# Kernel tuning notes

Measured on AMD Instinct MI355X. Metric: run time of the kernel, lower is better.

## Reference

```python
import jax, jax.numpy as jnp
import numpy as np

S_SCALE = 64.0   # arcface scale
MARGIN = 0.5     # arcface additive angular margin
EMB = 512
NUM_CLASSES = 100000
BATCH = 512


def setup_inputs() -> dict:
    key = jax.random.key(0)
    k1, k2, k3, k4 = jax.random.split(key, 4)
    # xavier_uniform for [num_classes, emb]
    limit = float(np.sqrt(6.0 / (NUM_CLASSES + EMB)))
    weight = jax.random.uniform(k1, (NUM_CLASSES, EMB), jnp.float32, -limit, limit)
    fc_weight = jax.random.uniform(k2, (NUM_CLASSES, EMB), jnp.float32, -limit, limit)
    local_embeddings = jax.random.normal(k3, (BATCH, EMB), jnp.float32)
    local_labels = jax.random.randint(k4, (BATCH,), 0, NUM_CLASSES, jnp.int64)
    return {
        "local_embeddings": local_embeddings,
        "weight": weight,
        "fc_weight": fc_weight,
        "local_labels": local_labels,
        "epoch": 40,
    }


def _l2norm(x, eps=1e-12):
    return x / jnp.maximum(jnp.linalg.norm(x, axis=-1, keepdims=True), eps)


def _arcface(logits, labels):
    # insightface ArcFace: replace target cosine with cos(theta + m), then scale by s
    rows = jnp.arange(logits.shape[0])
    target = logits[rows, labels]
    sin = jnp.sqrt(jnp.maximum(1.0 - target * target, 0.0))
    cos_m, sin_m = jnp.cos(MARGIN), jnp.sin(MARGIN)
    with_margin = target * cos_m - sin * sin_m            # cos(theta + m)
    # safeguard: only apply when theta + m <= pi  (target > cos(pi - m))
    threshold = jnp.cos(jnp.pi - MARGIN)
    mm = jnp.sin(jnp.pi - MARGIN) * MARGIN
    new_target = jnp.where(target > threshold, with_margin, target - mm)
    logits = logits.at[rows, labels].set(new_target)
    return logits * S_SCALE


def _ce(logits, labels):
    rows = jnp.arange(logits.shape[0])
    logp = jax.nn.log_softmax(logits, axis=-1)
    return -jnp.mean(logp[rows, labels])


def reference(local_embeddings, weight, fc_weight, local_labels, epoch):
    labels = local_labels.astype(jnp.int32)
    # margin branch: normalize both sides, cosine logits, arcface margin, CE
    norm_emb = _l2norm(local_embeddings)
    norm_w = _l2norm(weight)
    logits = norm_emb @ norm_w.T                   # [B, num_classes]
    logits = _arcface(logits, labels)
    margin_loss = _ce(logits, labels)
    # plain CE branch on raw linear
    ce_logits = local_embeddings @ fc_weight.T     # [B, num_classes]
    ce_loss = _ce(ce_logits, labels)
    if epoch <= 30:
        return ce_loss + 0.0 * margin_loss
    else:
        return 0.0 * ce_loss + margin_loss
```

## Files before the change

### kernel.cpp

```cpp
#include <hip/hip_runtime.h>

typedef __bf16 bf16x8 __attribute__((ext_vector_type(8)));
typedef float floatx4 __attribute__((ext_vector_type(4)));
typedef unsigned short ushortx8 __attribute__((ext_vector_type(8)));
typedef unsigned short ushort_t;

#define NC      100000
#define NCP     100096
#define EMBD    512
#define BATCH   512
#define BM      256
#define BN      128
#define BK      32
#define NCH     782

#define COS_M   0.8775825618903728f
#define SIN_M   0.479425538604203f
#define THRESH  (-0.8775825618903728f)
#define MM_C    0.2397127693021015f

__device__ __forceinline__ ushort_t f2bf(float f) {
  __bf16 h = (__bf16)f;
  return __builtin_bit_cast(ushort_t, h);
}

#define GLOAD16(g, l) __builtin_amdgcn_global_load_lds( \
    (const __attribute__((address_space(1))) void*)(g), \
    (__attribute__((address_space(3))) void*)(l), 16, 0, 0)

__global__ __launch_bounds__(256) void prep_small_k(
    const float* __restrict__ emb, const float* __restrict__ weight,
    const float* __restrict__ fcw, const int* __restrict__ labels,
    const int* __restrict__ epoch, ushort_t* __restrict__ Abf,
    float* __restrict__ tsc, int* __restrict__ lab32,
    float* __restrict__ out) {
  const bool mm = (*epoch > 30);
  const int tid = threadIdx.x;
  const int pred = (labels[2 * tid + 1] != 0) ? 1 : 0;
  const bool is64 = (__syncthreads_or(pred) == 0);

  const int w = tid >> 6, lane = tid & 63;
  const int row = blockIdx.x * 4 + w;
  const int lab = is64 ? labels[2 * row] : labels[row];
  const float* W = mm ? weight : fcw;

  const float* er = emb + (size_t)row * EMBD + lane * 8;
  const float* wr = W + (size_t)lab * EMBD + lane * 8;
  float4 e0 = *(const float4*)er,  e1 = *(const float4*)(er + 4);
  float4 w0 = *(const float4*)wr,  w1 = *(const float4*)(wr + 4);
  float dot = e0.x*w0.x + e0.y*w0.y + e0.z*w0.z + e0.w*w0.w
            + e1.x*w1.x + e1.y*w1.y + e1.z*w1.z + e1.w*w1.w;
  float ssa = e0.x*e0.x + e0.y*e0.y + e0.z*e0.z + e0.w*e0.w
            + e1.x*e1.x + e1.y*e1.y + e1.z*e1.z + e1.w*e1.w;
  float ssw = w0.x*w0.x + w0.y*w0.y + w0.z*w0.z + w0.w*w0.w
            + w1.x*w1.x + w1.y*w1.y + w1.z*w1.z + w1.w*w1.w;
  #pragma unroll
  for (int off = 32; off; off >>= 1) {
    dot += __shfl_xor(dot, off, 64);
    ssa += __shfl_xor(ssa, off, 64);
    ssw += __shfl_xor(ssw, off, 64);
  }
  const float inva = mm ? (1.0f / fmaxf(sqrtf(ssa), 1e-12f)) : 1.0f;
  ushortx8 o;
  o[0] = f2bf(e0.x*inva); o[1] = f2bf(e0.y*inva); o[2] = f2bf(e0.z*inva); o[3] = f2bf(e0.w*inva);
  o[4] = f2bf(e1.x*inva); o[5] = f2bf(e1.y*inva); o[6] = f2bf(e1.z*inva); o[7] = f2bf(e1.w*inva);
  *(ushortx8*)(Abf + (size_t)row * EMBD + lane * 8) = o;

  if (lane == 0) {
    lab32[row] = lab;
    float tv;
    if (mm) {
      float cosv = dot / (fmaxf(sqrtf(ssa), 1e-12f) * fmaxf(sqrtf(ssw), 1e-12f));
      float sinv = sqrtf(fmaxf(1.0f - cosv * cosv, 0.0f));
      float wmarg = cosv * COS_M - sinv * SIN_M;
      float nt = (cosv > THRESH) ? wmarg : (cosv - MM_C);
      tv = 64.0f * nt;
    } else {
      tv = dot;
    }
    tsc[row] = tv;
  }
  if (blockIdx.x == 0 && tid == 0) out[0] = 0.0f;
}

__global__ __launch_bounds__(256) void prep_w_k(
    const float* __restrict__ weight, const float* __restrict__ fcw,
    const int* __restrict__ epoch, ushort_t* __restrict__ Wbf) {
  const bool mm = (*epoch > 30);
  const float* W = mm ? weight : fcw;
  const int w = threadIdx.x >> 6, lane = threadIdx.x & 63;
  const int row = blockIdx.x * 4 + w;
  ushort_t* dst = Wbf + (size_t)row * EMBD + lane * 8;
  if (row >= NC) {
    *(ushortx8*)dst = (ushortx8)0;
    return;
  }
  const float* src = W + (size_t)row * EMBD + lane * 8;
  float4 a = *(const float4*)src;
  float4 b = *(const float4*)(src + 4);
  float ss = a.x*a.x + a.y*a.y + a.z*a.z + a.w*a.w
           + b.x*b.x + b.y*b.y + b.z*b.z + b.w*b.w;
  #pragma unroll
  for (int off = 32; off; off >>= 1) ss += __shfl_xor(ss, off, 64);
  const float inv = mm ? (1.0f / fmaxf(sqrtf(ss), 1e-12f)) : 1.0f;
  ushortx8 o;
  o[0] = f2bf(a.x*inv); o[1] = f2bf(a.y*inv); o[2] = f2bf(a.z*inv); o[3] = f2bf(a.w*inv);
  o[4] = f2bf(b.x*inv); o[5] = f2bf(b.y*inv); o[6] = f2bf(b.z*inv); o[7] = f2bf(b.w*inv);
  *(ushortx8*)dst = o;
}

__global__ __launch_bounds__(256, 2) void gemm_fused_k(
    const ushort_t* __restrict__ Abf, const ushort_t* __restrict__ Wbf,
    const float* __restrict__ tsc, const int* __restrict__ lab32,
    const int* __restrict__ epoch, float2* __restrict__ partials) {
  const int g = blockIdx.x >> 4, t = blockIdx.x & 15;
  const int bn = g * 8 + (t & 7);
  const int bm = t >> 3;
  if (bn >= NCH) return;

  const bool mm = (*epoch > 30);
  const float scale = mm ? 64.0f : 1.0f;

  __shared__ ushort_t As[BM * BK];
  __shared__ ushort_t Bs[BN * BK];
  __shared__ float tscS[BM];
  __shared__ int   labS[BM];

  const int tid  = threadIdx.x;
  const int lane = tid & 63;
  const int w    = tid >> 6;
  const int wm   = w * 64;
  const int m0   = bm * BM;
  const int n0   = bn * BN;

  tscS[tid] = tsc[m0 + tid];
  labS[tid] = lab32[m0 + tid];

  floatx4 acc[4][8];
  #pragma unroll
  for (int i = 0; i < 4; i++)
    #pragma unroll
    for (int j = 0; j < 8; j++) acc[i][j] = (floatx4){0.f, 0.f, 0.f, 0.f};

  const int r_in = lane >> 2;
  const int k_in = (lane & 3) * 8;
  const ushort_t* gA[4];
  ushort_t* lA[4];
  #pragma unroll
  for (int s = 0; s < 4; s++) {
    gA[s] = Abf + (size_t)(m0 + wm + s * 16 + r_in) * EMBD + k_in;
    lA[s] = &As[(wm + s * 16) * BK + lane * 8];
  }
  const ushort_t* gB[2];
  ushort_t* lB[2];
  #pragma unroll
  for (int s = 0; s < 2; s++) {
    gB[s] = Wbf + (size_t)(n0 + w * 32 + s * 16 + r_in) * EMBD + k_in;
    lB[s] = &Bs[(w * 32 + s * 16) * BK + lane * 8];
  }

  const int koff = (lane >> 4) * 8;
  const int rsel = lane & 15;

  for (int kt = 0; kt < EMBD / BK; ++kt) {
    #pragma unroll
    for (int s = 0; s < 4; s++) GLOAD16(gA[s] + kt * BK, lA[s]);
    #pragma unroll
    for (int s = 0; s < 2; s++) GLOAD16(gB[s] + kt * BK, lB[s]);
    __syncthreads();

    bf16x8 af[4], bv[8];
    #pragma unroll
    for (int mi = 0; mi < 4; mi++)
      af[mi] = *(const bf16x8*)&As[(wm + mi * 16 + rsel) * BK + koff];
    #pragma unroll
    for (int ni = 0; ni < 8; ni++)
      bv[ni] = *(const bf16x8*)&Bs[(ni * 16 + rsel) * BK + koff];
    #pragma unroll
    for (int mi = 0; mi < 4; mi++)
      #pragma unroll
      for (int ni = 0; ni < 8; ni++)
        acc[mi][ni] = __builtin_amdgcn_mfma_f32_16x16x32_bf16(
            af[mi], bv[ni], acc[mi][ni], 0, 0, 0);
    __syncthreads();
  }

  const int colq = lane & 15;
  const int rowq = lane >> 4;
  #pragma unroll
  for (int mi = 0; mi < 4; mi++) {
    #pragma unroll
    for (int r = 0; r < 4; r++) {
      const int rl = wm + mi * 16 + rowq * 4 + r;
      const int lab = labS[rl];
      const float tv = tscS[rl];
      float v[8];
      #pragma unroll
      for (int ni = 0; ni < 8; ni++) {
        const int cg = n0 + ni * 16 + colq;
        float x = acc[mi][ni][r] * scale;
        if (cg >= NC) x = -1e30f;
        else if (cg == lab) x = tv;
        v[ni] = x;
      }
      float mx = v[0];
      #pragma unroll
      for (int ni = 1; ni < 8; ni++) mx = fmaxf(mx, v[ni]);
      #pragma unroll
      for (int off = 1; off < 16; off <<= 1) mx = fmaxf(mx, __shfl_xor(mx, off, 64));
      float s = 0.0f;
      #pragma unroll
      for (int ni = 0; ni < 8; ni++) s += __expf(v[ni] - mx);
      #pragma unroll
      for (int off = 1; off < 16; off <<= 1) s += __shfl_xor(s, off, 64);
      if (colq == 0)
        partials[(size_t)(m0 + rl) * NCH + bn] = make_float2(mx, s);
    }
  }
}

__global__ __launch_bounds__(256) void rowmerge_k(
    const float2* __restrict__ partials, const float* __restrict__ tsc,
    float* __restrict__ out) {
  const int row = blockIdx.x;
  const int tid = threadIdx.x;
  float M = -1e30f, S = 0.0f;
  for (int j = tid; j < NCH; j += 256) {
    const float2 p = partials[(size_t)row * NCH + j];
    if (p.x > M) { S = S * __expf(M - p.x) + p.y; M = p.x; }
    else         { S += p.y * __expf(p.x - M); }
  }
  __shared__ float sm[256], sv[256];
  sm[tid] = M; sv[tid] = S;
  __syncthreads();
  for (int st = 128; st > 0; st >>= 1) {
    if (tid < st) {
      const float m2 = sm[tid + st], s2 = sv[tid + st];
      const float m1 = sm[tid],      s1 = sv[tid];
      const float Mn = fmaxf(m1, m2);
      sv[tid] = s1 * __expf(m1 - Mn) + s2 * __expf(m2 - Mn);
      sm[tid] = Mn;
    }
    __syncthreads();
  }
  if (tid == 0) {
    const float loss = (sm[0] + __logf(sv[0])) - tsc[row];
    atomicAdd(out, loss * (1.0f / 512.0f));
  }
}

extern "C" void kernel_launch(void* const* d_in, const int* in_sizes, int n_in,
                              void* d_out, int out_size, void* d_ws, size_t ws_size,
                              hipStream_t stream) {
  const float* emb    = (const float*)d_in[0];
  const float* weight = (const float*)d_in[1];
  const float* fcw    = (const float*)d_in[2];
  const int*   labels = (const int*)d_in[3];
  const int*   epoch  = (const int*)d_in[4];
  float* out = (float*)d_out;

  char* ws = (char*)d_ws;
  size_t off = 0;
  ushort_t* Abf = (ushort_t*)(ws + off); off += (size_t)BATCH * EMBD * 2;
  ushort_t* Wbf = (ushort_t*)(ws + off); off += (size_t)NCP * EMBD * 2;
  float* tsc       = (float*)(ws + off); off += BATCH * 4;
  int* lab32       = (int*)(ws + off);   off += BATCH * 4;
  float2* partials = (float2*)(ws + off); off += (size_t)BATCH * NCH * 8;

  prep_small_k<<<BATCH / 4, 256, 0, stream>>>(emb, weight, fcw, labels, epoch,
                                              Abf, tsc, lab32, out);
  prep_w_k<<<NCP / 4, 256, 0, stream>>>(weight, fcw, epoch, Wbf);
  gemm_fused_k<<<98 * 16, 256, 0, stream>>>(Abf, Wbf, tsc, lab32, epoch, partials);
  rowmerge_k<<<BATCH, 256, 0, stream>>>(partials, tsc, out);
}
```

Measured before the change: 473.5 us.

## Quantize operands to FP8 and use scaled f8f6f4 MFMA with swizzled LDS tiles

Embeddings and class weights are now converted to FP8 (e4m3) instead of bf16 in the prep kernels. The GEMM uses the 16x16x128 scaled f8f6f4 MFMA with unit scales. It takes K in 128-wide chunks through XOR-swizzled LDS and shrinks the M tile to 128, doubling the grid. This halves weight-staging traffic and raises matrix throughput, but coarser FP8 rounding of the cosine logits risks accuracy.

```diff
diff --git a/kernel.cpp b/kernel.cpp
--- a/kernel.cpp
+++ b/kernel.cpp
@@ -1,17 +1,13 @@
 #include <hip/hip_runtime.h>
 
-typedef __bf16 bf16x8 __attribute__((ext_vector_type(8)));
 typedef float floatx4 __attribute__((ext_vector_type(4)));
-typedef unsigned short ushortx8 __attribute__((ext_vector_type(8)));
-typedef unsigned short ushort_t;
+typedef int   intx4   __attribute__((ext_vector_type(4)));
+typedef int   intx8   __attribute__((ext_vector_type(8)));
 
 #define NC      100000
 #define NCP     100096
 #define EMBD    512
 #define BATCH   512
-#define BM      256
-#define BN      128
-#define BK      32
 #define NCH     782
 
 #define COS_M   0.8775825618903728f
@@ -19,19 +15,23 @@
 #define THRESH  (-0.8775825618903728f)
 #define MM_C    0.2397127693021015f
 
-__device__ __forceinline__ ushort_t f2bf(float f) {
-  __bf16 h = (__bf16)f;
-  return __builtin_bit_cast(ushort_t, h);
-}
-
 #define GLOAD16(g, l) __builtin_amdgcn_global_load_lds( \
     (const __attribute__((address_space(1))) void*)(g), \
     (__attribute__((address_space(3))) void*)(l), 16, 0, 0)
 
+__device__ __forceinline__ uint2 pack8_fp8(float4 a, float4 b) {
+  int lo = 0, hi = 0;
+  lo = __builtin_amdgcn_cvt_pk_fp8_f32(a.x, a.y, lo, false);
+  lo = __builtin_amdgcn_cvt_pk_fp8_f32(a.z, a.w, lo, true);
+  hi = __builtin_amdgcn_cvt_pk_fp8_f32(b.x, b.y, hi, false);
+  hi = __builtin_amdgcn_cvt_pk_fp8_f32(b.z, b.w, hi, true);
+  return make_uint2((unsigned)lo, (unsigned)hi);
+}
+
 __global__ __launch_bounds__(256) void prep_small_k(
     const float* __restrict__ emb, const float* __restrict__ weight,
     const float* __restrict__ fcw, const int* __restrict__ labels,
-    const int* __restrict__ epoch, ushort_t* __restrict__ Abf,
+    const int* __restrict__ epoch, unsigned char* __restrict__ Aq,
     float* __restrict__ tsc, int* __restrict__ lab32,
     float* __restrict__ out) {
   const bool mm = (*epoch > 30);
@@ -61,10 +61,9 @@
     ssw += __shfl_xor(ssw, off, 64);
   }
   const float inva = mm ? (1.0f / fmaxf(sqrtf(ssa), 1e-12f)) : 1.0f;
-  ushortx8 o;
-  o[0] = f2bf(e0.x*inva); o[1] = f2bf(e0.y*inva); o[2] = f2bf(e0.z*inva); o[3] = f2bf(e0.w*inva);
-  o[4] = f2bf(e1.x*inva); o[5] = f2bf(e1.y*inva); o[6] = f2bf(e1.z*inva); o[7] = f2bf(e1.w*inva);
-  *(ushortx8*)(Abf + (size_t)row * EMBD + lane * 8) = o;
+  float4 q0 = make_float4(e0.x*inva, e0.y*inva, e0.z*inva, e0.w*inva);
+  float4 q1 = make_float4(e1.x*inva, e1.y*inva, e1.z*inva, e1.w*inva);
+  *(uint2*)(Aq + (size_t)row * EMBD + lane * 8) = pack8_fp8(q0, q1);
 
   if (lane == 0) {
     lab32[row] = lab;
@@ -85,14 +84,14 @@
 
 __global__ __launch_bounds__(256) void prep_w_k(
     const float* __restrict__ weight, const float* __restrict__ fcw,
-    const int* __restrict__ epoch, ushort_t* __restrict__ Wbf) {
+    const int* __restrict__ epoch, unsigned char* __restrict__ Wq) {
   const bool mm = (*epoch > 30);
   const float* W = mm ? weight : fcw;
   const int w = threadIdx.x >> 6, lane = threadIdx.x & 63;
   const int row = blockIdx.x * 4 + w;
-  ushort_t* dst = Wbf + (size_t)row * EMBD + lane * 8;
+  unsigned char* dst = Wq + (size_t)row * EMBD + lane * 8;
   if (row >= NC) {
-    *(ushortx8*)dst = (ushortx8)0;
+    *(uint2*)dst = make_uint2(0u, 0u);
     return;
   }
   const float* src = W + (size_t)row * EMBD + lane * 8;
@@ -103,95 +102,96 @@
   #pragma unroll
   for (int off = 32; off; off >>= 1) ss += __shfl_xor(ss, off, 64);
   const float inv = mm ? (1.0f / fmaxf(sqrtf(ss), 1e-12f)) : 1.0f;
-  ushortx8 o;
-  o[0] = f2bf(a.x*inv); o[1] = f2bf(a.y*inv); o[2] = f2bf(a.z*inv); o[3] = f2bf(a.w*inv);
-  o[4] = f2bf(b.x*inv); o[5] = f2bf(b.y*inv); o[6] = f2bf(b.z*inv); o[7] = f2bf(b.w*inv);
-  *(ushortx8*)dst = o;
+  float4 qa = make_float4(a.x*inv, a.y*inv, a.z*inv, a.w*inv);
+  float4 qb = make_float4(b.x*inv, b.y*inv, b.z*inv, b.w*inv);
+  *(uint2*)dst = pack8_fp8(qa, qb);
 }
 
 __global__ __launch_bounds__(256, 2) void gemm_fused_k(
-    const ushort_t* __restrict__ Abf, const ushort_t* __restrict__ Wbf,
+    const unsigned char* __restrict__ Aq, const unsigned char* __restrict__ Wq,
     const float* __restrict__ tsc, const int* __restrict__ lab32,
     const int* __restrict__ epoch, float2* __restrict__ partials) {
-  const int g = blockIdx.x >> 4, t = blockIdx.x & 15;
-  const int bn = g * 8 + (t & 7);
+  const int t = blockIdx.x & 31, gblk = blockIdx.x >> 5;
+  const int bn = gblk * 8 + (t & 7);
   const int bm = t >> 3;
   if (bn >= NCH) return;
 
   const bool mm = (*epoch > 30);
   const float scale = mm ? 64.0f : 1.0f;
 
-  __shared__ ushort_t As[BM * BK];
-  __shared__ ushort_t Bs[BN * BK];
-  __shared__ float tscS[BM];
-  __shared__ int   labS[BM];
+  __shared__ unsigned char As[128 * 128];
+  __shared__ unsigned char Bs[128 * 128];
+  __shared__ float tscS[128];
+  __shared__ int   labS[128];
 
   const int tid  = threadIdx.x;
   const int lane = tid & 63;
   const int w    = tid >> 6;
-  const int wm   = w * 64;
-  const int m0   = bm * BM;
-  const int n0   = bn * BN;
-
-  tscS[tid] = tsc[m0 + tid];
-  labS[tid] = lab32[m0 + tid];
-
-  floatx4 acc[4][8];
-  #pragma unroll
-  for (int i = 0; i < 4; i++)
+  const int m0   = bm * 128;
+  const int n0   = bn * 128;
+
+  if (tid < 128) { tscS[tid] = tsc[m0 + tid]; labS[tid] = lab32[m0 + tid]; }
+
+  floatx4 acc[2][8];
+  #pragma unroll
+  for (int i = 0; i < 2; i++)
     #pragma unroll
     for (int j = 0; j < 8; j++) acc[i][j] = (floatx4){0.f, 0.f, 0.f, 0.f};
 
-  const int r_in = lane >> 2;
-  const int k_in = (lane & 3) * 8;
-  const ushort_t* gA[4];
-  ushort_t* lA[4];
+  const int rseg = lane >> 3;
+  const int swz  = ((lane & 7) ^ rseg) * 16;
+  const unsigned char* gA[4];
+  const unsigned char* gB[4];
   #pragma unroll
   for (int s = 0; s < 4; s++) {
-    gA[s] = Abf + (size_t)(m0 + wm + s * 16 + r_in) * EMBD + k_in;
-    lA[s] = &As[(wm + s * 16) * BK + lane * 8];
-  }
-  const ushort_t* gB[2];
-  ushort_t* lB[2];
-  #pragma unroll
-  for (int s = 0; s < 2; s++) {
-    gB[s] = Wbf + (size_t)(n0 + w * 32 + s * 16 + r_in) * EMBD + k_in;
-    lB[s] = &Bs[(w * 32 + s * 16) * BK + lane * 8];
-  }
-
-  const int koff = (lane >> 4) * 8;
+    gA[s] = Aq + (size_t)(m0 + w * 32 + s * 8 + rseg) * EMBD + swz;
+    gB[s] = Wq + (size_t)(n0 + w * 32 + s * 8 + rseg) * EMBD + swz;
+  }
+
   const int rsel = lane & 15;
-
-  for (int kt = 0; kt < EMBD / BK; ++kt) {
-    #pragma unroll
-    for (int s = 0; s < 4; s++) GLOAD16(gA[s] + kt * BK, lA[s]);
-    #pragma unroll
-    for (int s = 0; s < 2; s++) GLOAD16(gB[s] + kt * BK, lB[s]);
+  const int g2   = (lane >> 4) * 2;
+  const int c0   = (g2 ^ (rsel & 7)) * 16;
+  const int c1   = ((g2 + 1) ^ (rsel & 7)) * 16;
+
+  for (int kt = 0; kt < 4; ++kt) {
+    #pragma unroll
+    for (int s = 0; s < 4; s++) {
+      GLOAD16(gA[s] + kt * 128, &As[(w * 32 + s * 8) * 128]);
+      GLOAD16(gB[s] + kt * 128, &Bs[(w * 32 + s * 8) * 128]);
+    }
     __syncthreads();
 
-    bf16x8 af[4], bv[8];
-    #pragma unroll
-    for (int mi = 0; mi < 4; mi++)
-      af[mi] = *(const bf16x8*)&As[(wm + mi * 16 + rsel) * BK + koff];
-    #pragma unroll
-    for (int ni = 0; ni < 8; ni++)
-      bv[ni] = *(const bf16x8*)&Bs[(ni * 16 + rsel) * BK + koff];
-    #pragma unroll
-    for (int mi = 0; mi < 4; mi++)
+    intx8 af[2], bv[8];
+    #pragma unroll
+    for (int mi = 0; mi < 2; mi++) {
+      const int base = (w * 32 + mi * 16 + rsel) * 128;
+      intx4 lo = *(const intx4*)&As[base + c0];
+      intx4 hi = *(const intx4*)&As[base + c1];
+      af[mi] = __builtin_shufflevector(lo, hi, 0, 1, 2, 3, 4, 5, 6, 7);
+    }
+    #pragma unroll
+    for (int ni = 0; ni < 8; ni++) {
+      const int base = (ni * 16 + rsel) * 128;
+      intx4 lo = *(const intx4*)&Bs[base + c0];
+      intx4 hi = *(const intx4*)&Bs[base + c1];
+      bv[ni] = __builtin_shufflevector(lo, hi, 0, 1, 2, 3, 4, 5, 6, 7);
+    }
+    #pragma unroll
+    for (int mi = 0; mi < 2; mi++)
       #pragma unroll
       for (int ni = 0; ni < 8; ni++)
-        acc[mi][ni] = __builtin_amdgcn_mfma_f32_16x16x32_bf16(
-            af[mi], bv[ni], acc[mi][ni], 0, 0, 0);
+        acc[mi][ni] = __builtin_amdgcn_mfma_scale_f32_16x16x128_f8f6f4(
+            af[mi], bv[ni], acc[mi][ni], 0, 0,
+            0, 0x7f7f7f7f, 0, 0x7f7f7f7f);
     __syncthreads();
   }
 
   const int colq = lane & 15;
-  const int rowq = lane >> 4;
-  #pragma unroll
-  for (int mi = 0; mi < 4; mi++) {
+  #pragma unroll
+  for (int mi = 0; mi < 2; mi++) {
     #pragma unroll
     for (int r = 0; r < 4; r++) {
-      const int rl = wm + mi * 16 + rowq * 4 + r;
+      const int rl = w * 32 + mi * 16 + (lane >> 4) * 4 + r;
       const int lab = labS[rl];
       const float tv = tscS[rl];
       float v[8];
@@ -261,15 +261,15 @@
 
   char* ws = (char*)d_ws;
   size_t off = 0;
-  ushort_t* Abf = (ushort_t*)(ws + off); off += (size_t)BATCH * EMBD * 2;
-  ushort_t* Wbf = (ushort_t*)(ws + off); off += (size_t)NCP * EMBD * 2;
+  unsigned char* Aq = (unsigned char*)(ws + off); off += (size_t)BATCH * EMBD;
+  unsigned char* Wq = (unsigned char*)(ws + off); off += (size_t)NCP * EMBD;
   float* tsc       = (float*)(ws + off); off += BATCH * 4;
   int* lab32       = (int*)(ws + off);   off += BATCH * 4;
   float2* partials = (float2*)(ws + off); off += (size_t)BATCH * NCH * 8;
 
   prep_small_k<<<BATCH / 4, 256, 0, stream>>>(emb, weight, fcw, labels, epoch,
-                                              Abf, tsc, lab32, out);
-  prep_w_k<<<NCP / 4, 256, 0, stream>>>(weight, fcw, epoch, Wbf);
-  gemm_fused_k<<<98 * 16, 256, 0, stream>>>(Abf, Wbf, tsc, lab32, epoch, partials);
+                                              Aq, tsc, lab32, out);
+  prep_w_k<<<NCP / 4, 256, 0, stream>>>(weight, fcw, epoch, Wq);
+  gemm_fused_k<<<98 * 32, 256, 0, stream>>>(Aq, Wq, tsc, lab32, epoch, partials);
   rowmerge_k<<<BATCH, 256, 0, stream>>>(partials, tsc, out);
 }
```

Measured after the change: 471.7 us. No clear change (-0.4%).
